# Kernel tuning notes

Hardware: AMD Instinct MI355X
Metric: run time of the kernel (lower is better)

Reference implementation:

```python
import jax, jax.numpy as jnp
import numpy as np

B, N, F_IN, OUT_DIM, H = 8, 2048, 128, 256, 4
D = OUT_DIM // H  # head dim = 64
NEG_SLOPE = 0.2


def setup_inputs() -> dict:
    key = jax.random.key(0)
    k_a, k_x, k_w, k_s, k_d = jax.random.split(key, 5)
    A = jax.random.randint(k_a, (B, N, N), 0, 2).astype(jnp.float32)
    # ensure self-loops so no softmax row is fully masked (-inf -> NaN)
    eye = jnp.eye(N, dtype=jnp.float32)
    A = jnp.maximum(A, eye[None, :, :])
    X = jax.random.normal(k_x, (B, N, F_IN), dtype=jnp.float32)
    # xavier-uniform-like scales
    w_lim = float(np.sqrt(6.0 / (F_IN + OUT_DIM)))
    a_lim = float(np.sqrt(6.0 / (H + D)))
    W = jax.random.uniform(k_w, (OUT_DIM, F_IN), minval=-w_lim, maxval=w_lim, dtype=jnp.float32)
    a_src = jax.random.uniform(k_s, (H, D), minval=-a_lim, maxval=a_lim, dtype=jnp.float32)
    a_dst = jax.random.uniform(k_d, (H, D), minval=-a_lim, maxval=a_lim, dtype=jnp.float32)
    return {"A": A, "X": X, "W": W, "a_src": a_src, "a_dst": a_dst}


def reference(A, X, W, a_src, a_dst):
    b, n, _ = X.shape
    h, d = a_src.shape
    # X_trans = W(X); torch Linear: X @ W.T, W: (out_dim, in_dim)
    X_split = (X @ W.T).reshape(b, n, h, d)  # (b, n, h, d)
    attn_src = jnp.einsum('bnhd,hd->bnh', X_split, a_src)
    attn_dst = jnp.einsum('bnhd,hd->bnh', X_split, a_dst)
    # (b, n, n, h) dense score tensor
    attn = attn_src[:, :, None, :] + attn_dst[:, None, :, :]
    attn = jnp.where(attn >= 0, attn, NEG_SLOPE * attn)  # leaky_relu(0.2)
    attn = jnp.where(A[..., None] == 0, -jnp.inf, attn)
    attn = jax.nn.softmax(attn, axis=2)
    # torch.einsum('bnnk,bnkd->bnkd') with repeated 'n' -> DIAGONAL of attn,
    # elementwise-scaled features (faithful to original code).
    diag = jnp.einsum('bnnh->bnh', attn)  # (b, n, h): self-attention weights
    out = (diag[..., None] * X_split).reshape(b, n, h * d)
    return out
```

## Files before the change

### kernel.cpp

```cpp
#include <hip/hip_runtime.h>
#include <hip/hip_bf16.h>

#define B_   8
#define N_   2048
#define FIN  128
#define OUTD 256
#define H_   4
#define LOG2E 1.44269504088896340736f

typedef __bf16 bf16x8 __attribute__((ext_vector_type(8)));
typedef float  f32x4  __attribute__((ext_vector_type(4)));

__global__ __launch_bounds__(256) void conv_bf16(const float* __restrict__ X,
                                                 const float* __restrict__ W,
                                                 unsigned short* __restrict__ Xb,
                                                 unsigned short* __restrict__ Wb) {
    const int NX4 = (B_ * N_ * FIN) / 4;
    int i = blockIdx.x * 256 + threadIdx.x;
    const float4* src;
    ushort4* dst;
    int idx;
    if (i < NX4) { src = (const float4*)X; dst = (ushort4*)Xb; idx = i; }
    else         { src = (const float4*)W; dst = (ushort4*)Wb; idx = i - NX4; }
    float4 v = src[idx];
    __hip_bfloat16 b0 = __float2bfloat16(v.x);
    __hip_bfloat16 b1 = __float2bfloat16(v.y);
    __hip_bfloat16 b2 = __float2bfloat16(v.z);
    __hip_bfloat16 b3 = __float2bfloat16(v.w);
    ushort4 o;
    o.x = *(unsigned short*)&b0;
    o.y = *(unsigned short*)&b1;
    o.z = *(unsigned short*)&b2;
    o.w = *(unsigned short*)&b3;
    dst[idx] = o;
}

__global__ __launch_bounds__(256) void gemm_bf16(const unsigned short* __restrict__ Xb,
                                                 const unsigned short* __restrict__ Wb,
                                                 float* __restrict__ Xt) {
    int r0   = blockIdx.x * 16;
    int wave = threadIdx.x >> 6;
    int lane = threadIdx.x & 63;
    int c0   = (blockIdx.y * 4 + wave) * 16;
    int m = lane & 15, q = lane >> 4;

    const bf16x8* Arow = (const bf16x8*)(Xb + (size_t)(r0 + m) * FIN);
    const bf16x8* Brow = (const bf16x8*)(Wb + (size_t)(c0 + m) * FIN);
    f32x4 acc = {0.f, 0.f, 0.f, 0.f};
#pragma unroll
    for (int kc = 0; kc < 4; ++kc) {
        bf16x8 af = Arow[kc * 4 + q];
        bf16x8 bf = Brow[kc * 4 + q];
        acc = __builtin_amdgcn_mfma_f32_16x16x32_bf16(af, bf, acc, 0, 0, 0);
    }
    float* outp = Xt + (size_t)(r0 + q * 4) * OUTD + c0 + m;
#pragma unroll
    for (int reg = 0; reg < 4; ++reg)
        outp[(size_t)reg * OUTD] = acc[reg];
}

__global__ __launch_bounds__(256) void st_kernel(const float* __restrict__ Xt,
                                                 const float* __restrict__ a_src,
                                                 const float* __restrict__ a_dst,
                                                 float* __restrict__ s_arr,
                                                 float* __restrict__ t_arr) {
    int row  = blockIdx.x * 4 + (threadIdx.x >> 6);
    int lane = threadIdx.x & 63;
    const float* xr = Xt + (size_t)row * OUTD;
#pragma unroll
    for (int h = 0; h < H_; ++h) {
        float v  = xr[h * 64 + lane];
        float vs = v * a_src[h * 64 + lane];
        float vd = v * a_dst[h * 64 + lane];
#pragma unroll
        for (int off = 32; off > 0; off >>= 1) {
            vs += __shfl_down(vs, off);
            vd += __shfl_down(vd, off);
        }
        if (lane == 0) {
            s_arr[(size_t)row * H_ + h] = vs * LOG2E;
            t_arr[(size_t)row * H_ + h] = vd * LOG2E;
        }
    }
}

__global__ __launch_bounds__(256) void gat_main(const float* __restrict__ A,
                                                const float* __restrict__ s_arr,
                                                const float* __restrict__ t_arr,
                                                float* __restrict__ out) {
    __shared__ float t_lds[N_ * H_];
    __shared__ float diag_lds[16][H_];

    int b  = blockIdx.x >> 7;
    int rt = blockIdx.x & 127;
    int r0 = rt * 16;
    int tid = threadIdx.x;

    {
        const float4* tsrc = (const float4*)(t_arr + (size_t)b * N_ * H_);
        float4* tdst = (float4*)t_lds;
        for (int i = tid; i < (N_ * H_) / 4; i += 256) tdst[i] = tsrc[i];
    }
    __syncthreads();

    int r  = tid >> 4;
    int lj = tid & 15;
    int gi = r0 + r;

    f32x4 s4 = *(const f32x4*)(s_arr + ((size_t)b * N_ + gi) * H_);
    const float* Arow = A + ((size_t)b * N_ + gi) * N_;

    float acc0 = 0.f, acc1 = 0.f, acc2 = 0.f, acc3 = 0.f;
    for (int it = 0; it < N_ / 64; ++it) {
        int j = it * 64 + lj * 4;
        float4 a4 = *(const float4*)(Arow + j);
#pragma unroll
        for (int jj = 0; jj < 4; ++jj) {
            f32x4 t4 = ((const f32x4*)t_lds)[j + jj];
            float aj = (jj == 0) ? a4.x : (jj == 1) ? a4.y : (jj == 2) ? a4.z : a4.w;
            float y0 = s4[0] + t4[0]; y0 = fmaxf(y0, 0.2f * y0); acc0 = fmaf(aj, exp2f(y0), acc0);
            float y1 = s4[1] + t4[1]; y1 = fmaxf(y1, 0.2f * y1); acc1 = fmaf(aj, exp2f(y1), acc1);
            float y2 = s4[2] + t4[2]; y2 = fmaxf(y2, 0.2f * y2); acc2 = fmaf(aj, exp2f(y2), acc2);
            float y3 = s4[3] + t4[3]; y3 = fmaxf(y3, 0.2f * y3); acc3 = fmaf(aj, exp2f(y3), acc3);
        }
    }
#pragma unroll
    for (int mk = 8; mk > 0; mk >>= 1) {
        acc0 += __shfl_xor(acc0, mk);
        acc1 += __shfl_xor(acc1, mk);
        acc2 += __shfl_xor(acc2, mk);
        acc3 += __shfl_xor(acc3, mk);
    }
    if (lj == 0) {
        f32x4 ti = ((const f32x4*)t_lds)[gi];
        float y, e;
        y = s4[0] + ti[0]; y = fmaxf(y, 0.2f * y); e = exp2f(y); diag_lds[r][0] = e / acc0;
        y = s4[1] + ti[1]; y = fmaxf(y, 0.2f * y); e = exp2f(y); diag_lds[r][1] = e / acc1;
        y = s4[2] + ti[2]; y = fmaxf(y, 0.2f * y); e = exp2f(y); diag_lds[r][2] = e / acc2;
        y = s4[3] + ti[3]; y = fmaxf(y, 0.2f * y); e = exp2f(y); diag_lds[r][3] = e / acc3;
    }
    __syncthreads();

    float* orow = out + ((size_t)b * N_ + gi) * OUTD;
#pragma unroll
    for (int ii = 0; ii < 4; ++ii) {
        int c = lj * 4 + ii * 64;
        float4 v = *(float4*)(orow + c);
        float dg = diag_lds[r][ii];
        v.x *= dg; v.y *= dg; v.z *= dg; v.w *= dg;
        *(float4*)(orow + c) = v;
    }
}

extern "C" void kernel_launch(void* const* d_in, const int* in_sizes, int n_in,
                              void* d_out, int out_size, void* d_ws, size_t ws_size,
                              hipStream_t stream) {
    const float* A     = (const float*)d_in[0];
    const float* X     = (const float*)d_in[1];
    const float* W     = (const float*)d_in[2];
    const float* a_src = (const float*)d_in[3];
    const float* a_dst = (const float*)d_in[4];
    float* out = (float*)d_out;

    char* ws = (char*)d_ws;
    unsigned short* Xb = (unsigned short*)ws;
    unsigned short* Wb = (unsigned short*)(ws + 4194304);
    float* s_arr = (float*)(ws + 4259840);
    float* t_arr = (float*)(ws + 4521984);

    conv_bf16<<<2080, 256, 0, stream>>>(X, W, Xb, Wb);
    gemm_bf16<<<dim3(1024, 4), 256, 0, stream>>>(Xb, Wb, out);
    st_kernel<<<4096, 256, 0, stream>>>(out, a_src, a_dst, s_arr, t_arr);
    gat_main<<<1024, 256, 0, stream>>>(A, s_arr, t_arr, out);
}
```

Measured before the change: 244.9 us.

## Vectorize score projection, prefetch adjacency loads, use raw exp2 intrinsic

```diff
diff --git a/kernel.cpp b/kernel.cpp
--- a/kernel.cpp
+++ b/kernel.cpp
@@ -66,21 +66,21 @@
                                                  float* __restrict__ t_arr) {
     int row  = blockIdx.x * 4 + (threadIdx.x >> 6);
     int lane = threadIdx.x & 63;
-    const float* xr = Xt + (size_t)row * OUTD;
+    f32x4 v  = ((const f32x4*)(Xt + (size_t)row * OUTD))[lane];
+    f32x4 as = ((const f32x4*)a_src)[lane];
+    f32x4 ad = ((const f32x4*)a_dst)[lane];
+
+    float vs = fmaf(v[0], as[0], fmaf(v[1], as[1], fmaf(v[2], as[2], v[3] * as[3])));
+    float vd = fmaf(v[0], ad[0], fmaf(v[1], ad[1], fmaf(v[2], ad[2], v[3] * ad[3])));
 #pragma unroll
-    for (int h = 0; h < H_; ++h) {
-        float v  = xr[h * 64 + lane];
-        float vs = v * a_src[h * 64 + lane];
-        float vd = v * a_dst[h * 64 + lane];
-#pragma unroll
-        for (int off = 32; off > 0; off >>= 1) {
-            vs += __shfl_down(vs, off);
-            vd += __shfl_down(vd, off);
-        }
-        if (lane == 0) {
-            s_arr[(size_t)row * H_ + h] = vs * LOG2E;
-            t_arr[(size_t)row * H_ + h] = vd * LOG2E;
-        }
+    for (int off = 1; off < 16; off <<= 1) {
+        vs += __shfl_xor(vs, off);
+        vd += __shfl_xor(vd, off);
+    }
+    if ((lane & 15) == 0) {
+        int h = lane >> 4;
+        s_arr[(size_t)row * H_ + h] = vs * LOG2E;
+        t_arr[(size_t)row * H_ + h] = vd * LOG2E;
     }
 }
 
@@ -99,7 +99,9 @@
     {
         const float4* tsrc = (const float4*)(t_arr + (size_t)b * N_ * H_);
         float4* tdst = (float4*)t_lds;
-        for (int i = tid; i < (N_ * H_) / 4; i += 256) tdst[i] = tsrc[i];
+#pragma unroll
+        for (int i = 0; i < (N_ * H_) / 4 / 256; ++i)
+            tdst[tid + i * 256] = tsrc[tid + i * 256];
     }
     __syncthreads();
 
@@ -110,34 +112,46 @@
     f32x4 s4 = *(const f32x4*)(s_arr + ((size_t)b * N_ + gi) * H_);
     const float* Arow = A + ((size_t)b * N_ + gi) * N_;
 
-    float acc0 = 0.f, acc1 = 0.f, acc2 = 0.f, acc3 = 0.f;
-    for (int it = 0; it < N_ / 64; ++it) {
+    f32x4 acc = {0.f, 0.f, 0.f, 0.f};
+
+    auto body = [&](float4 a4, int it) {
         int j = it * 64 + lj * 4;
-        float4 a4 = *(const float4*)(Arow + j);
 #pragma unroll
         for (int jj = 0; jj < 4; ++jj) {
             f32x4 t4 = ((const f32x4*)t_lds)[j + jj];
             float aj = (jj == 0) ? a4.x : (jj == 1) ? a4.y : (jj == 2) ? a4.z : a4.w;
-            float y0 = s4[0] + t4[0]; y0 = fmaxf(y0, 0.2f * y0); acc0 = fmaf(aj, exp2f(y0), acc0);
-            float y1 = s4[1] + t4[1]; y1 = fmaxf(y1, 0.2f * y1); acc1 = fmaf(aj, exp2f(y1), acc1);
-            float y2 = s4[2] + t4[2]; y2 = fmaxf(y2, 0.2f * y2); acc2 = fmaf(aj, exp2f(y2), acc2);
-            float y3 = s4[3] + t4[3]; y3 = fmaxf(y3, 0.2f * y3); acc3 = fmaf(aj, exp2f(y3), acc3);
+#pragma unroll
+            for (int h = 0; h < H_; ++h) {
+                float y = s4[h] + t4[h];
+                y = fmaxf(y, 0.2f * y);
+                acc[h] = fmaf(aj, __builtin_amdgcn_exp2f(y), acc[h]);
+            }
         }
+    };
+
+    float4 a4 = *(const float4*)(Arow + lj * 4);
+    for (int it = 0; it < 31; ++it) {
+        float4 a4n = *(const float4*)(Arow + (it + 1) * 64 + lj * 4);
+        body(a4, it);
+        a4 = a4n;
     }
+    body(a4, 31);
+
 #pragma unroll
     for (int mk = 8; mk > 0; mk >>= 1) {
-        acc0 += __shfl_xor(acc0, mk);
-        acc1 += __shfl_xor(acc1, mk);
-        acc2 += __shfl_xor(acc2, mk);
-        acc3 += __shfl_xor(acc3, mk);
+        acc[0] += __shfl_xor(acc[0], mk);
+        acc[1] += __shfl_xor(acc[1], mk);
+        acc[2] += __shfl_xor(acc[2], mk);
+        acc[3] += __shfl_xor(acc[3], mk);
     }
     if (lj == 0) {
         f32x4 ti = ((const f32x4*)t_lds)[gi];
-        float y, e;
-        y = s4[0] + ti[0]; y = fmaxf(y, 0.2f * y); e = exp2f(y); diag_lds[r][0] = e / acc0;
-        y = s4[1] + ti[1]; y = fmaxf(y, 0.2f * y); e = exp2f(y); diag_lds[r][1] = e / acc1;
-        y = s4[2] + ti[2]; y = fmaxf(y, 0.2f * y); e = exp2f(y); diag_lds[r][2] = e / acc2;
-        y = s4[3] + ti[3]; y = fmaxf(y, 0.2f * y); e = exp2f(y); diag_lds[r][3] = e / acc3;
+#pragma unroll
+        for (int h = 0; h < H_; ++h) {
+            float y = s4[h] + ti[h];
+            y = fmaxf(y, 0.2f * y);
+            diag_lds[r][h] = __builtin_amdgcn_exp2f(y) / acc[h];
+        }
     }
     __syncthreads();
 
```

New measurement: 236.4 us. -3.4%, faster.
